# Performance work log

Hardware: AMD Instinct MI355X
Metric: run time of the kernel (lower is better)

## Reference

```python
import jax, jax.numpy as jnp
import numpy as np

PAD = 0

def setup_inputs() -> dict:
    key = jax.random.key(0)
    ks = jax.random.split(key, 16)
    B, S, D, F = 64, 512, 768, 256
    VOCAB = 32000
    # variable-length tweets: length in [8, S], rest is padding (token id PAD=0)
    lengths = jax.random.randint(ks[0], (B,), 8, S + 1)
    tok = jax.random.randint(ks[1], (B, S), 1, VOCAB)
    x = jnp.where(jnp.arange(S)[None, :] < lengths[:, None], tok, PAD)
    h = jax.random.normal(ks[2], (B, S, D), dtype=jnp.float32)
    sc = 0.02
    w2 = jax.random.normal(ks[3], (F, D, 2), dtype=jnp.float32) * sc
    b2 = jax.random.normal(ks[4], (F,), dtype=jnp.float32) * sc
    w3 = jax.random.normal(ks[5], (F, D, 3), dtype=jnp.float32) * sc
    b3 = jax.random.normal(ks[6], (F,), dtype=jnp.float32) * sc
    w4 = jax.random.normal(ks[7], (F, D, 4), dtype=jnp.float32) * sc
    b4 = jax.random.normal(ks[8], (F,), dtype=jnp.float32) * sc
    w5 = jax.random.normal(ks[9], (F, D, 5), dtype=jnp.float32) * sc
    b5 = jax.random.normal(ks[10], (F,), dtype=jnp.float32) * sc
    fc_w = jax.random.normal(ks[11], (1, 4 * F), dtype=jnp.float32) * sc
    fc_b = jax.random.normal(ks[12], (1,), dtype=jnp.float32) * sc
    return {"x": x, "h": h, "w2": w2, "b2": b2, "w3": w3, "b3": b3,
            "w4": w4, "b4": b4, "w5": w5, "b5": b5, "fc_w": fc_w, "fc_b": fc_b}


def _branch(hc, L, w, b):
    # hc: [B, D, S] front-compacted hidden states; w: [F, D, k]
    k = w.shape[-1]
    out = jax.lax.conv_general_dilated(
        hc, w, window_strides=(1,), padding='VALID',
        dimension_numbers=('NCH', 'OIH', 'NCH')) + b[None, :, None]  # [B,F,S-k+1]
    T = out.shape[-1]
    # conv position t is valid iff t + k - 1 < L  <=>  t < L - k + 1
    valid = jnp.arange(T)[None, :] < (L - k + 1)[:, None]           # [B,T]
    neg = jnp.asarray(-jnp.inf, out.dtype)
    pooled = jnp.max(jnp.where(valid[:, None, :], out, neg), axis=-1)  # [B,F]
    return jax.nn.relu(pooled)


def reference(x, h, w2, b2, w3, b3, w4, b4, w5, b5, fc_w, fc_b):
    mask = x != PAD                                   # [B,S]
    L = mask.sum(axis=1)                              # [B]
    # stable compaction: move non-pad token hidden states to the front, order preserved
    order = jnp.argsort(jnp.logical_not(mask), axis=1, stable=True)   # [B,S]
    hc = jnp.take_along_axis(h, order[..., None], axis=1)             # [B,S,D]
    hc = hc.transpose(0, 2, 1)                                        # [B,D,S]
    feats = jnp.concatenate([
        _branch(hc, L, w2, b2),
        _branch(hc, L, w3, b3),
        _branch(hc, L, w4, b4),
        _branch(hc, L, w5, b5),
    ], axis=-1)                                       # [B, 4F]
    logits = feats @ fc_w.T + fc_b                    # [B,1]
    return jax.nn.sigmoid(logits).squeeze(-1)         # [B]
```

## Files before the change

### kernel.cpp

```cpp
#include <hip/hip_runtime.h>
#include <stdint.h>

#define Bn 64
#define Sn 512
#define SPn 520
#define Dn 768
#define JSTRIDE 196608
#define ABUF 16640
#define BSLOT 8192
#define QS_A 28.222222f
#define SAQ 0.035433072f

typedef int iv4 __attribute__((ext_vector_type(4)));

static __device__ __forceinline__ signed char q8(float f, float s) {
  float t = __builtin_rintf(f * s);
  t = fmaxf(-127.f, fminf(127.f, t));
  return (signed char)(int)t;
}

static __device__ __forceinline__ void gload16(const void* g, void* l) {
  __builtin_amdgcn_global_load_lds(
      (const __attribute__((address_space(1))) unsigned int*)g,
      (__attribute__((address_space(3))) unsigned int*)l, 16, 0, 0);
}

template<int N> __device__ __forceinline__ void waitv() {
  static_assert(N == 0 || N == 1 || N == 4, "");
  if constexpr (N == 0) asm volatile("s_waitcnt vmcnt(0)" ::: "memory");
  else if constexpr (N == 1) asm volatile("s_waitcnt vmcnt(1)" ::: "memory");
  else asm volatile("s_waitcnt vmcnt(4)" ::: "memory");
}

__global__ __launch_bounds__(256) void plan_kernel(
    const int* __restrict__ x, int* __restrict__ plan, int* __restrict__ rowmap) {
  __shared__ int sL[64];
  __shared__ int sOff[65];
  int tid = threadIdx.x, lane = tid & 63, wv = tid >> 6;
  for (int bb = wv; bb < 64; bb += 4) {
    int cnt = 0;
    for (int c = 0; c < 8; ++c) {
      unsigned long long m = __ballot(x[bb * Sn + c * 64 + lane] != 0);
      cnt += __popcll(m);
    }
    if (lane == 0) sL[bb] = cnt;
  }
  __syncthreads();
  if (tid < 64) {
    int L = sL[tid];
    int SL = (L + 15) & ~15;
    int pre = SL;
    #pragma unroll
    for (int off = 1; off < 64; off <<= 1) {
      int y = __shfl_up(pre, off);
      if (tid >= off) pre += y;
    }
    sOff[tid] = pre - SL;
    if (tid == 63) { sOff[64] = pre; plan[0] = (pre + 255) >> 8; }
  }
  __syncthreads();
  int M = sOff[64];
  for (int b = 0; b < 64; ++b) {
    int off = sOff[b], L = sL[b];
    int SL = (L + 15) & ~15;
    int enc = (b << 20) | (L << 10);
    for (int t = tid; t < SL; t += 256) rowmap[off + t] = enc | t;
  }
  for (int p = M + tid; p < M + 264; p += 256)
    rowmap[p] = 512;
}

__global__ __launch_bounds__(256) void stage_kernel(
    const int* __restrict__ x, const float* __restrict__ h,
    const float* __restrict__ w2, const float* __restrict__ w3,
    const float* __restrict__ w4, const float* __restrict__ w5,
    signed char* __restrict__ hcq, signed char* __restrict__ wq,
    float* __restrict__ fscale) {
  int tid = threadIdx.x, lane = tid & 63, wv = tid >> 6;
  if (blockIdx.x < 512) {
    int cidx = blockIdx.x;
    int b = cidx >> 3, rblk = cidx & 7;
    __shared__ unsigned long long masks[8];
    __shared__ short sidx[Sn];
    for (int c = wv; c < 8; c += 4) {
      unsigned long long m = __ballot(x[b * Sn + c * 64 + lane] != 0);
      if (lane == 0) masks[c] = m;
    }
    __syncthreads();
    int pref[9]; pref[0] = 0;
    #pragma unroll
    for (int c = 0; c < 8; ++c) pref[c + 1] = pref[c] + __popcll(masks[c]);
    int L = pref[8];
    for (int p = tid; p < Sn; p += 256) {
      int c = p >> 6, l = p & 63;
      unsigned long long m = masks[c];
      if ((m >> l) & 1ull)
        sidx[pref[c] + __popcll(m & ((1ull << l) - 1ull))] = (short)p;
    }
    __syncthreads();
    int r0 = rblk * 65;
    for (int r = r0 + wv; r < r0 + 65; r += 4) {
      if (r < L) {
        signed char* dst = hcq + ((size_t)b * SPn + r) * Dn;
        const float* src = h + ((size_t)b * Sn + sidx[r]) * Dn;
        #pragma unroll
        for (int c = 0; c < 3; ++c) {
          int d = c * 256 + lane * 4;
          float4 v = *(const float4*)(src + d);
          char4 o = { q8(v.x, QS_A), q8(v.y, QS_A), q8(v.z, QS_A), q8(v.w, QS_A) };
          *(char4*)(dst + d) = o;
        }
      }
    }
  } else {
    __shared__ float sf[3840];
    __shared__ float smax[4];
    int bb = blockIdx.x - 512;
    int br = bb >> 8, f = bb & 255, k = br + 2;
    const float* w = (br == 0) ? w2 : (br == 1) ? w3 : (br == 2) ? w4 : w5;
    int mBase = 256 * ((br * (br + 3)) >> 1);
    const float* src = w + (size_t)f * Dn * k;
    int n = Dn * k;
    float mx = 0.f;
    for (int e = tid; e < n; e += 256) {
      float v = src[e];
      sf[e] = v;
      mx = fmaxf(mx, fabsf(v));
    }
    #pragma unroll
    for (int off = 32; off; off >>= 1) mx = fmaxf(mx, __shfl_xor(mx, off));
    if (lane == 0) smax[wv] = mx;
    __syncthreads();
    float M = fmaxf(fmaxf(smax[0], smax[1]), fmaxf(smax[2], smax[3]));
    M = fmaxf(M, 1e-30f);
    if (tid == 0) fscale[br * 256 + f] = M / 127.f;
    float qs = 127.f / M;
    for (int j = 0; j < k; ++j) {
      signed char* dst = wq + (size_t)(mBase + j * 256 + f) * Dn;
      for (int d = tid; d < Dn; d += 256) dst[d] = q8(sf[d * k + j], qs);
    }
  }
}

static __device__ __forceinline__ void issueA(
    int d0i, char* sA, const char* const (&gA)[2], const char* gAt,
    int lane, int wvoff) {
  int aoff = (d0i + 1) * 64;
  char* nA = sA + ((d0i + 1) & 1) * ABUF;
  #pragma unroll
  for (int p = 0; p < 2; ++p) gload16(gA[p] + aoff, nA + p * 8192 + wvoff);
  if (lane < 16) gload16(gAt + aoff, nA + 16384);
}

template<int J, int W, int J2, int DADD, int DOA>
static __device__ __forceinline__ void conv_step(
    int d0i, int bsl0, char* sA, char* sB,
    const char* const (&gA)[2], const char* gAt, const char* gB0,
    int lane, int wr, int wc, int lrow, int lg, int wvoff, iv4 (&acc)[4][4]) {
  int sl = bsl0 + J;      sl  -= (sl  >= 3) ? 3 : 0; sl  -= (sl  >= 3) ? 3 : 0;
  int dsl = bsl0 + J + 2; dsl -= (dsl >= 3) ? 3 : 0; dsl -= (dsl >= 3) ? 3 : 0;
  {
    int boff = J2 * JSTRIDE + (d0i + DADD) * 64;
    gload16(gB0 + boff, sB + dsl * BSLOT + wvoff);
  }
  if constexpr (DOA) issueA(d0i, sA, gA, gAt, lane, wvoff);
  const char* curA = sA + (d0i & 1) * ABUF;
  const char* curB = sB + sl * BSLOT;
  iv4 Af[4], Bf[4];
  #pragma unroll
  for (int m = 0; m < 4; ++m) {
    int row = wr * 64 + m * 16 + lrow + J;
    Af[m] = *(const iv4*)(curA + row * 64 + ((lg ^ ((row >> 1) & 3)) << 4));
  }
  #pragma unroll
  for (int n = 0; n < 4; ++n) {
    int row = wc * 64 + n * 16 + lrow;
    Bf[n] = *(const iv4*)(curB + row * 64 + ((lg ^ ((row >> 1) & 3)) << 4));
  }
  __builtin_amdgcn_s_setprio(1);
  #pragma unroll
  for (int n = 0; n < 4; ++n)
    #pragma unroll
    for (int m = 0; m < 4; ++m)
      acc[m][n] = __builtin_amdgcn_mfma_i32_16x16x64_i8(Af[m], Bf[n], acc[m][n], 0, 0, 0);
  __builtin_amdgcn_s_setprio(0);
  __builtin_amdgcn_sched_barrier(0);
  waitv<W>();
  __builtin_amdgcn_sched_barrier(0);
  __builtin_amdgcn_s_barrier();
  __builtin_amdgcn_sched_barrier(0);
}

#define SA bsl0, sA, sB, gA, gAt, gB0, lane, wr, wc, lrow, lg, wvoff, acc

template<int KK>
static __device__ __forceinline__ void conv_loop(
    char* sA, char* sB, const char* const (&gA)[2], const char* gAt,
    const char* gB0,
    int lane, int wr, int wc, int lrow, int lg, int wvoff, iv4 (&acc)[4][4]) {
  #pragma unroll
  for (int p = 0; p < 2; ++p) gload16(gA[p], sA + p * 8192 + wvoff);
  if (lane < 16) gload16(gAt, sA + 16384);
  gload16(gB0, sB + wvoff);
  gload16(gB0 + JSTRIDE, sB + BSLOT + wvoff);
  __builtin_amdgcn_sched_barrier(0);
  waitv<1>();
  __builtin_amdgcn_sched_barrier(0);
  __builtin_amdgcn_s_barrier();
  __builtin_amdgcn_sched_barrier(0);
  int bsl0 = 0;
  for (int d0i = 0; d0i < 11; ++d0i) {
    if constexpr (KK == 5) {
      conv_step<0,4,2,0,1>(d0i, SA);
      conv_step<1,4,3,0,0>(d0i, SA);
      conv_step<2,1,4,0,0>(d0i, SA);
      conv_step<3,1,0,1,0>(d0i, SA);
      conv_step<4,1,1,1,0>(d0i, SA);
    } else if constexpr (KK == 4) {
      conv_step<0,4,2,0,1>(d0i, SA);
      conv_step<1,4,3,0,0>(d0i, SA);
      conv_step<2,1,0,1,0>(d0i, SA);
      conv_step<3,1,1,1,0>(d0i, SA);
    } else if constexpr (KK == 3) {
      conv_step<0,4,2,0,1>(d0i, SA);
      conv_step<1,4,0,1,0>(d0i, SA);
      conv_step<2,1,1,1,0>(d0i, SA);
    } else {
      conv_step<0,4,0,1,1>(d0i, SA);
      conv_step<1,1,1,1,0>(d0i, SA);
    }
    bsl0 += KK; bsl0 -= (bsl0 >= 3) ? 3 : 0; bsl0 -= (bsl0 >= 3) ? 3 : 0;
  }
  if constexpr (KK == 5) {
    conv_step<0,1,2,0,0>(11, SA);
    conv_step<1,1,3,0,0>(11, SA);
    conv_step<2,1,4,0,0>(11, SA);
    conv_step<3,1,0,1,0>(11, SA);
    conv_step<4,1,1,1,0>(11, SA);
  } else if constexpr (KK == 4) {
    conv_step<0,1,2,0,0>(11, SA);
    conv_step<1,1,3,0,0>(11, SA);
    conv_step<2,1,0,1,0>(11, SA);
    conv_step<3,1,1,1,0>(11, SA);
  } else if constexpr (KK == 3) {
    conv_step<0,1,2,0,0>(11, SA);
    conv_step<1,1,0,1,0>(11, SA);
    conv_step<2,1,1,1,0>(11, SA);
  } else {
    conv_step<0,1,0,1,0>(11, SA);
    conv_step<1,1,1,1,0>(11, SA);
  }
  waitv<0>();
}

__global__ __launch_bounds__(512, 4) void conv_kernel(
    const signed char* __restrict__ hcq, const signed char* __restrict__ wq,
    const float* __restrict__ b2, const float* __restrict__ b3,
    const float* __restrict__ b4, const float* __restrict__ b5,
    const float* __restrict__ fscale,
    const int* __restrict__ plan, const int* __restrict__ rowmap,
    int* __restrict__ feats) {
  __shared__ char smem[2 * ABUF + 3 * BSLOT];
  char* sA = smem;
  char* sB = smem + 2 * ABUF;
  int idx = blockIdx.x;
  int xcd = idx & 7, s2 = idx >> 3;
  int sub = s2 & 7, tile = xcd + ((s2 >> 3) << 3);
  if (tile >= plan[0]) return;
  int br = 3 - (sub >> 1), ff = sub & 1, kk = br + 2;
  int mBase = 256 * ((br * (br + 3)) >> 1) + ff * 128;
  const float* bias = (br == 0) ? b2 : (br == 1) ? b3 : (br == 2) ? b4 : b5;
  int tid = threadIdx.x, lane = tid & 63, wv = tid >> 6;
  int wr = wv >> 1, wc = wv & 1;
  int lrow = lane & 15, lg = lane >> 4;
  int wvoff = wv * 1024;
  int P0 = tile << 8;

  const char* gA[2];
  #pragma unroll
  for (int p = 0; p < 2; ++p) {
    int c = p * 512 + tid;
    int row = c >> 2, sgp = c & 3;
    int rm = rowmap[P0 + row];
    int bb_ = rm >> 20, t = rm & 1023;
    int seg = sgp ^ ((row >> 1) & 3);
    gA[p] = (const char*)(hcq + ((size_t)(bb_ * SPn + t)) * Dn + seg * 16);
  }
  const char* gAt;
  {
    int l = lane & 15;
    int row = 256 + (l >> 2), sgp = l & 3;
    int rm = rowmap[P0 + row];
    int bb_ = rm >> 20, t = rm & 1023;
    int seg = sgp ^ ((row >> 1) & 3);
    gAt = (const char*)(hcq + ((size_t)(bb_ * SPn + t)) * Dn + seg * 16);
  }
  const char* gB0;
  {
    int row = tid >> 2, sgp = tid & 3;
    int seg = sgp ^ ((row >> 1) & 3);
    gB0 = (const char*)(wq + ((size_t)(mBase + row)) * Dn + seg * 16);
  }

  iv4 acc[4][4];
  #pragma unroll
  for (int m = 0; m < 4; ++m)
    #pragma unroll
    for (int n = 0; n < 4; ++n) acc[m][n] = (iv4)0;

  switch (br) {
    case 3: conv_loop<5>(sA, sB, gA, gAt, gB0, lane, wr, wc, lrow, lg, wvoff, acc); break;
    case 2: conv_loop<4>(sA, sB, gA, gAt, gB0, lane, wr, wc, lrow, lg, wvoff, acc); break;
    case 1: conv_loop<3>(sA, sB, gA, gAt, gB0, lane, wr, wc, lrow, lg, wvoff, acc); break;
    default: conv_loop<2>(sA, sB, gA, gAt, gB0, lane, wr, wc, lrow, lg, wvoff, acc); break;
  }

  int rmv[4];
  #pragma unroll
  for (int m = 0; m < 4; ++m) rmv[m] = rowmap[P0 + wr * 64 + m * 16];
  #pragma unroll
  for (int n = 0; n < 4; ++n) {
    int fg = ff * 128 + wc * 64 + n * 16 + lrow;
    float bv = bias[fg];
    float sfc = fscale[br * 256 + fg] * SAQ;
    #pragma unroll
    for (int m = 0; m < 4; ++m) {
      int bb_ = rmv[m] >> 20;
      int Lb = (rmv[m] >> 10) & 1023;
      int t0 = (rmv[m] & 1023) + lg * 4;
      int vlim = Lb - kk + 1;
      float pmax = 0.f;
      #pragma unroll
      for (int i = 0; i < 4; ++i) {
        float v = (float)acc[m][n][i] * sfc + bv;
        pmax = fmaxf(pmax, (t0 + i < vlim) ? fmaxf(v, 0.f) : 0.f);
      }
      pmax = fmaxf(pmax, __shfl_xor(pmax, 16));
      pmax = fmaxf(pmax, __shfl_xor(pmax, 32));
      if (lane < 16 && pmax > 0.f)
        atomicMax(feats + bb_ * 1024 + br * 256 + fg, __float_as_int(pmax));
    }
  }
}

__global__ __launch_bounds__(64) void fc_kernel(
    const int* __restrict__ feats, const float* __restrict__ fcw,
    const float* __restrict__ fcb, float* __restrict__ out) {
  int b = blockIdx.x, lane = threadIdx.x;
  float acc = 0.f;
  for (int i = lane; i < 1024; i += 64)
    acc += __int_as_float(feats[b * 1024 + i]) * fcw[i];
  #pragma unroll
  for (int off = 32; off; off >>= 1) acc += __shfl_xor(acc, off);
  if (lane == 0) out[b] = 1.f / (1.f + expf(-(acc + fcb[0])));
}

extern "C" void kernel_launch(void* const* d_in, const int* in_sizes, int n_in,
                              void* d_out, int out_size, void* d_ws, size_t ws_size,
                              hipStream_t stream) {
  const int*   x   = (const int*)d_in[0];
  const float* h   = (const float*)d_in[1];
  const float* w2  = (const float*)d_in[2];
  const float* b2  = (const float*)d_in[3];
  const float* w3  = (const float*)d_in[4];
  const float* b3  = (const float*)d_in[5];
  const float* w4  = (const float*)d_in[6];
  const float* b4  = (const float*)d_in[7];
  const float* w5  = (const float*)d_in[8];
  const float* b5  = (const float*)d_in[9];
  const float* fcw = (const float*)d_in[10];
  const float* fcb = (const float*)d_in[11];
  float* out = (float*)d_out;
  char* ws = (char*)d_ws;
  signed char* hcq = (signed char*)ws;
  signed char* wq  = (signed char*)(ws + 25559040);
  float* fscale = (float*)(ws + 28311552);
  int* feats  = (int*)(ws + 28315648);
  int* plan   = (int*)(ws + 28577792);
  int* rowmap = (int*)(ws + 28577808);

  hipMemsetAsync(feats, 0, 64 * 1024 * 4, stream);
  plan_kernel<<<1, 256, 0, stream>>>(x, plan, rowmap);
  stage_kernel<<<1536, 256, 0, stream>>>(x, h, w2, w3, w4, w5, hcq, wq, fscale);
  conv_kernel<<<1024, 512, 0, stream>>>(hcq, wq, b2, b3, b4, b5, fscale, plan, rowmap, feats);
  fc_kernel<<<64, 64, 0, stream>>>(feats, fcw, fcb, out);
}
```

Measured before the change: 115.2 us.

## Double-buffer register fragments and deepen B ring to four LDS slots

The conv main loop is restructured so each step prefetches the next step's A/B fragments from LDS into a second register set while the MFMAs on the current set run, and the B staging ring grows from three to four slots with power-of-two indexing. Launch bounds drop from 4 to 2 blocks per CU to make room for the extra fragment registers. Separately, the feats memset moves into plan_kernel, and weight quantization stores are vectorized to char4. The cost is more VGPRs and LDS, which may lower occupancy, in exchange for hiding LDS read latency and removing one launch.

```diff
diff --git a/kernel.cpp b/kernel.cpp
--- a/kernel.cpp
+++ b/kernel.cpp
@@ -32,11 +32,21 @@
   else asm volatile("s_waitcnt vmcnt(4)" ::: "memory");
 }
 
+template<int S, typename T, int N>
+static __device__ __forceinline__ T (&sel(T (&a)[N], T (&b)[N]))[N] {
+  if constexpr (S) return b; else return a;
+}
+
 __global__ __launch_bounds__(256) void plan_kernel(
-    const int* __restrict__ x, int* __restrict__ plan, int* __restrict__ rowmap) {
+    const int* __restrict__ x, int* __restrict__ plan, int* __restrict__ rowmap,
+    int* __restrict__ feats) {
   __shared__ int sL[64];
   __shared__ int sOff[65];
   int tid = threadIdx.x, lane = tid & 63, wv = tid >> 6;
+  {
+    int4 z = {0, 0, 0, 0};
+    for (int i = tid * 4; i < 65536; i += 1024) *(int4*)(feats + i) = z;
+  }
   for (int bb = wv; bb < 64; bb += 4) {
     int cnt = 0;
     for (int c = 0; c < 8; ++c) {
@@ -137,7 +147,11 @@
     float qs = 127.f / M;
     for (int j = 0; j < k; ++j) {
       signed char* dst = wq + (size_t)(mBase + j * 256 + f) * Dn;
-      for (int d = tid; d < Dn; d += 256) dst[d] = q8(sf[d * k + j], qs);
+      for (int d4 = tid * 4; d4 < Dn; d4 += 1024) {
+        char4 o = { q8(sf[(d4 + 0) * k + j], qs), q8(sf[(d4 + 1) * k + j], qs),
+                    q8(sf[(d4 + 2) * k + j], qs), q8(sf[(d4 + 3) * k + j], qs) };
+        *(char4*)(dst + d4) = o;
+      }
     }
   }
 }
@@ -152,31 +166,8 @@
   if (lane < 16) gload16(gAt + aoff, nA + 16384);
 }
 
-template<int J, int W, int J2, int DADD, int DOA>
-static __device__ __forceinline__ void conv_step(
-    int d0i, int bsl0, char* sA, char* sB,
-    const char* const (&gA)[2], const char* gAt, const char* gB0,
-    int lane, int wr, int wc, int lrow, int lg, int wvoff, iv4 (&acc)[4][4]) {
-  int sl = bsl0 + J;      sl  -= (sl  >= 3) ? 3 : 0; sl  -= (sl  >= 3) ? 3 : 0;
-  int dsl = bsl0 + J + 2; dsl -= (dsl >= 3) ? 3 : 0; dsl -= (dsl >= 3) ? 3 : 0;
-  {
-    int boff = J2 * JSTRIDE + (d0i + DADD) * 64;
-    gload16(gB0 + boff, sB + dsl * BSLOT + wvoff);
-  }
-  if constexpr (DOA) issueA(d0i, sA, gA, gAt, lane, wvoff);
-  const char* curA = sA + (d0i & 1) * ABUF;
-  const char* curB = sB + sl * BSLOT;
-  iv4 Af[4], Bf[4];
-  #pragma unroll
-  for (int m = 0; m < 4; ++m) {
-    int row = wr * 64 + m * 16 + lrow + J;
-    Af[m] = *(const iv4*)(curA + row * 64 + ((lg ^ ((row >> 1) & 3)) << 4));
-  }
-  #pragma unroll
-  for (int n = 0; n < 4; ++n) {
-    int row = wc * 64 + n * 16 + lrow;
-    Bf[n] = *(const iv4*)(curB + row * 64 + ((lg ^ ((row >> 1) & 3)) << 4));
-  }
+static __device__ __forceinline__ void domfma(
+    iv4 (&Af)[4], iv4 (&Bf)[4], iv4 (&acc)[4][4]) {
   __builtin_amdgcn_s_setprio(1);
   #pragma unroll
   for (int n = 0; n < 4; ++n)
@@ -184,6 +175,40 @@
     for (int m = 0; m < 4; ++m)
       acc[m][n] = __builtin_amdgcn_mfma_i32_16x16x64_i8(Af[m], Bf[n], acc[m][n], 0, 0, 0);
   __builtin_amdgcn_s_setprio(0);
+}
+
+static __device__ __forceinline__ void gates_(int W4) {}
+
+template<int J, int W, int J3, int DADD, int DOA, int SET, int PRE, int PJ, int PDADD>
+static __device__ __forceinline__ void stepN(
+    int d0i, int bsl0, char* sA, char* sB,
+    const char* const (&gA)[2], const char* gAt, const char* gB0,
+    int lane, int wr, int wc, int lrow, int lg, int wvoff,
+    iv4 (&Af0)[4], iv4 (&Bf0)[4], iv4 (&Af1)[4], iv4 (&Bf1)[4],
+    iv4 (&acc)[4][4]) {
+  {
+    int dsl = (bsl0 + J + 3) & 3;
+    gload16(gB0 + J3 * JSTRIDE + (d0i + DADD) * 64, sB + dsl * BSLOT + wvoff);
+  }
+  if constexpr (DOA) issueA(d0i, sA, gA, gAt, lane, wvoff);
+  if constexpr (PRE) {
+    int psl = (bsl0 + J + 1) & 3;
+    const char* pA = sA + ((d0i + PDADD) & 1) * ABUF;
+    const char* pB = sB + psl * BSLOT;
+    iv4 (&Afn)[4] = sel<(SET ^ 1)>(Af0, Af1);
+    iv4 (&Bfn)[4] = sel<(SET ^ 1)>(Bf0, Bf1);
+    #pragma unroll
+    for (int n = 0; n < 4; ++n) {
+      int row = wc * 64 + n * 16 + lrow;
+      Bfn[n] = *(const iv4*)(pB + row * 64 + ((lg ^ ((row >> 1) & 3)) << 4));
+    }
+    #pragma unroll
+    for (int m = 0; m < 4; ++m) {
+      int row = wr * 64 + m * 16 + lrow + PJ;
+      Afn[m] = *(const iv4*)(pA + row * 64 + ((lg ^ ((row >> 1) & 3)) << 4));
+    }
+  }
+  domfma(sel<SET>(Af0, Af1), sel<SET>(Bf0, Bf1), acc);
   __builtin_amdgcn_sched_barrier(0);
   waitv<W>();
   __builtin_amdgcn_sched_barrier(0);
@@ -191,76 +216,153 @@
   __builtin_amdgcn_sched_barrier(0);
 }
 
-#define SA bsl0, sA, sB, gA, gAt, gB0, lane, wr, wc, lrow, lg, wvoff, acc
+template<int J, int W, int J3, int DADD, int DOA, int SET, int PRE>
+static __device__ __forceinline__ void step2(
+    int d0i, int bsl0, char* sA, char* sB,
+    const char* const (&gA)[2], const char* gAt, const char* gB0,
+    int lane, int wr, int wc, int lrow, int lg, int wvoff,
+    iv4 (&Bf0)[4], iv4 (&Bf1)[4], iv4 (&acc)[4][4]) {
+  {
+    int dsl = (bsl0 + J + 3) & 3;
+    gload16(gB0 + J3 * JSTRIDE + (d0i + DADD) * 64, sB + dsl * BSLOT + wvoff);
+  }
+  if constexpr (DOA) issueA(d0i, sA, gA, gAt, lane, wvoff);
+  const char* pA = sA + (d0i & 1) * ABUF;
+  iv4 Af[4];
+  #pragma unroll
+  for (int m = 0; m < 4; ++m) {
+    int row = wr * 64 + m * 16 + lrow + J;
+    Af[m] = *(const iv4*)(pA + row * 64 + ((lg ^ ((row >> 1) & 3)) << 4));
+  }
+  if constexpr (PRE) {
+    int psl = (bsl0 + J + 1) & 3;
+    const char* pB = sB + psl * BSLOT;
+    iv4 (&Bfn)[4] = sel<(SET ^ 1)>(Bf0, Bf1);
+    #pragma unroll
+    for (int n = 0; n < 4; ++n) {
+      int row = wc * 64 + n * 16 + lrow;
+      Bfn[n] = *(const iv4*)(pB + row * 64 + ((lg ^ ((row >> 1) & 3)) << 4));
+    }
+  }
+  domfma(Af, sel<SET>(Bf0, Bf1), acc);
+  __builtin_amdgcn_sched_barrier(0);
+  waitv<W>();
+  __builtin_amdgcn_sched_barrier(0);
+  __builtin_amdgcn_s_barrier();
+  __builtin_amdgcn_sched_barrier(0);
+}
+
+#define SN bsl0, sA, sB, gA, gAt, gB0, lane, wr, wc, lrow, lg, wvoff, Af0, Bf0, Af1, Bf1, acc
+#define S2 bsl0, sA, sB, gA, gAt, gB0, lane, wr, wc, lrow, lg, wvoff, Bf0, Bf1, acc
 
 template<int KK>
 static __device__ __forceinline__ void conv_loop(
     char* sA, char* sB, const char* const (&gA)[2], const char* gAt,
     const char* gB0,
     int lane, int wr, int wc, int lrow, int lg, int wvoff, iv4 (&acc)[4][4]) {
+  iv4 Af0[4], Bf0[4], Af1[4], Bf1[4];
   #pragma unroll
   for (int p = 0; p < 2; ++p) gload16(gA[p], sA + p * 8192 + wvoff);
   if (lane < 16) gload16(gAt, sA + 16384);
   gload16(gB0, sB + wvoff);
   gload16(gB0 + JSTRIDE, sB + BSLOT + wvoff);
-  __builtin_amdgcn_sched_barrier(0);
-  waitv<1>();
+  constexpr int OFF2 = (KK >= 3) ? 2 * JSTRIDE : 64;
+  gload16(gB0 + OFF2, sB + 2 * BSLOT + wvoff);
+  __builtin_amdgcn_sched_barrier(0);
+  waitv<0>();
   __builtin_amdgcn_sched_barrier(0);
   __builtin_amdgcn_s_barrier();
   __builtin_amdgcn_sched_barrier(0);
+  {
+    #pragma unroll
+    for (int n = 0; n < 4; ++n) {
+      int row = wc * 64 + n * 16 + lrow;
+      Bf0[n] = *(const iv4*)(sB + row * 64 + ((lg ^ ((row >> 1) & 3)) << 4));
+    }
+    if constexpr (KK >= 3) {
+      #pragma unroll
+      for (int m = 0; m < 4; ++m) {
+        int row = wr * 64 + m * 16 + lrow;
+        Af0[m] = *(const iv4*)(sA + row * 64 + ((lg ^ ((row >> 1) & 3)) << 4));
+      }
+    }
+  }
   int bsl0 = 0;
-  for (int d0i = 0; d0i < 11; ++d0i) {
-    if constexpr (KK == 5) {
-      conv_step<0,4,2,0,1>(d0i, SA);
-      conv_step<1,4,3,0,0>(d0i, SA);
-      conv_step<2,1,4,0,0>(d0i, SA);
-      conv_step<3,1,0,1,0>(d0i, SA);
-      conv_step<4,1,1,1,0>(d0i, SA);
-    } else if constexpr (KK == 4) {
-      conv_step<0,4,2,0,1>(d0i, SA);
-      conv_step<1,4,3,0,0>(d0i, SA);
-      conv_step<2,1,0,1,0>(d0i, SA);
-      conv_step<3,1,1,1,0>(d0i, SA);
-    } else if constexpr (KK == 3) {
-      conv_step<0,4,2,0,1>(d0i, SA);
-      conv_step<1,4,0,1,0>(d0i, SA);
-      conv_step<2,1,1,1,0>(d0i, SA);
-    } else {
-      conv_step<0,4,0,1,1>(d0i, SA);
-      conv_step<1,1,1,1,0>(d0i, SA);
-    }
-    bsl0 += KK; bsl0 -= (bsl0 >= 3) ? 3 : 0; bsl0 -= (bsl0 >= 3) ? 3 : 0;
-  }
   if constexpr (KK == 5) {
-    conv_step<0,1,2,0,0>(11, SA);
-    conv_step<1,1,3,0,0>(11, SA);
-    conv_step<2,1,4,0,0>(11, SA);
-    conv_step<3,1,0,1,0>(11, SA);
-    conv_step<4,1,1,1,0>(11, SA);
+    for (int dd = 0; dd < 10; dd += 2) {
+      stepN<0,4,3,0,1, 0,1,1,0>(dd, SN);
+      stepN<1,4,4,0,0, 1,1,2,0>(dd, SN);
+      stepN<2,1,0,1,0, 0,1,3,0>(dd, SN);
+      stepN<3,1,1,1,0, 1,1,4,0>(dd, SN);
+      stepN<4,1,2,1,0, 0,1,0,1>(dd, SN);
+      bsl0 = (bsl0 + 5) & 3;
+      stepN<0,4,3,0,1, 1,1,1,0>(dd + 1, SN);
+      stepN<1,4,4,0,0, 0,1,2,0>(dd + 1, SN);
+      stepN<2,1,0,1,0, 1,1,3,0>(dd + 1, SN);
+      stepN<3,1,1,1,0, 0,1,4,0>(dd + 1, SN);
+      stepN<4,1,2,1,0, 1,1,0,1>(dd + 1, SN);
+      bsl0 = (bsl0 + 5) & 3;
+    }
+    stepN<0,4,3,0,1, 0,1,1,0>(10, SN);
+    stepN<1,4,4,0,0, 1,1,2,0>(10, SN);
+    stepN<2,1,0,1,0, 0,1,3,0>(10, SN);
+    stepN<3,1,1,1,0, 1,1,4,0>(10, SN);
+    stepN<4,1,2,1,0, 0,1,0,1>(10, SN);
+    bsl0 = (bsl0 + 5) & 3;
+    stepN<0,1,3,0,0, 1,1,1,0>(11, SN);
+    stepN<1,1,4,0,0, 0,1,2,0>(11, SN);
+    stepN<2,1,0,1,0, 1,1,3,0>(11, SN);
+    stepN<3,1,1,1,0, 0,1,4,0>(11, SN);
+    stepN<4,1,2,1,0, 1,0,0,0>(11, SN);
   } else if constexpr (KK == 4) {
-    conv_step<0,1,2,0,0>(11, SA);
-    conv_step<1,1,3,0,0>(11, SA);
-    conv_step<2,1,0,1,0>(11, SA);
-    conv_step<3,1,1,1,0>(11, SA);
+    for (int dd = 0; dd < 11; ++dd) {
+      stepN<0,4,3,0,1, 0,1,1,0>(dd, SN);
+      stepN<1,4,0,1,0, 1,1,2,0>(dd, SN);
+      stepN<2,1,1,1,0, 0,1,3,0>(dd, SN);
+      stepN<3,1,2,1,0, 1,1,0,1>(dd, SN);
+    }
+    stepN<0,1,3,0,0, 0,1,1,0>(11, SN);
+    stepN<1,1,0,1,0, 1,1,2,0>(11, SN);
+    stepN<2,1,1,1,0, 0,1,3,0>(11, SN);
+    stepN<3,1,2,1,0, 1,0,0,0>(11, SN);
   } else if constexpr (KK == 3) {
-    conv_step<0,1,2,0,0>(11, SA);
-    conv_step<1,1,0,1,0>(11, SA);
-    conv_step<2,1,1,1,0>(11, SA);
+    for (int dd = 0; dd < 10; dd += 2) {
+      stepN<0,4,0,1,1, 0,1,1,0>(dd, SN);
+      stepN<1,1,1,1,0, 1,1,2,0>(dd, SN);
+      stepN<2,1,2,1,0, 0,1,0,1>(dd, SN);
+      bsl0 = (bsl0 + 3) & 3;
+      stepN<0,4,0,1,1, 1,1,1,0>(dd + 1, SN);
+      stepN<1,1,1,1,0, 0,1,2,0>(dd + 1, SN);
+      stepN<2,1,2,1,0, 1,1,0,1>(dd + 1, SN);
+      bsl0 = (bsl0 + 3) & 3;
+    }
+    stepN<0,4,0,1,1, 0,1,1,0>(10, SN);
+    stepN<1,1,1,1,0, 1,1,2,0>(10, SN);
+    stepN<2,1,2,1,0, 0,1,0,1>(10, SN);
+    bsl0 = (bsl0 + 3) & 3;
+    stepN<0,1,0,1,0, 1,1,1,0>(11, SN);
+    stepN<1,1,1,1,0, 0,1,2,0>(11, SN);
+    stepN<2,1,2,1,0, 1,0,0,0>(11, SN);
   } else {
-    conv_step<0,1,0,1,0>(11, SA);
-    conv_step<1,1,1,1,0>(11, SA);
+    for (int dd = 0; dd < 11; ++dd) {
+      step2<0,4,1,1,1, 0,1>(dd, S2);
+      step2<1,1,0,2,0, 1,1>(dd, S2);
+      bsl0 = (bsl0 + 2) & 3;
+    }
+    step2<0,1,1,1,0, 0,1>(11, S2);
+    step2<1,1,0,2,0, 1,0>(11, S2);
   }
   waitv<0>();
 }
 
-__global__ __launch_bounds__(512, 4) void conv_kernel(
+__global__ __launch_bounds__(512, 2) void conv_kernel(
     const signed char* __restrict__ hcq, const signed char* __restrict__ wq,
     const float* __restrict__ b2, const float* __restrict__ b3,
     const float* __restrict__ b4, const float* __restrict__ b5,
     const float* __restrict__ fscale,
     const int* __restrict__ plan, const int* __restrict__ rowmap,
     int* __restrict__ feats) {
-  __shared__ char smem[2 * ABUF + 3 * BSLOT];
+  __shared__ char smem[2 * ABUF + 4 * BSLOT];
   char* sA = smem;
   char* sB = smem + 2 * ABUF;
   int idx = blockIdx.x;
@@ -379,8 +481,7 @@
   int* plan   = (int*)(ws + 28577792);
   int* rowmap = (int*)(ws + 28577808);
 
-  hipMemsetAsync(feats, 0, 64 * 1024 * 4, stream);
-  plan_kernel<<<1, 256, 0, stream>>>(x, plan, rowmap);
+  plan_kernel<<<1, 256, 0, stream>>>(x, plan, rowmap, feats);
   stage_kernel<<<1536, 256, 0, stream>>>(x, h, w2, w3, w4, w5, hcq, wq, fscale);
   conv_kernel<<<1024, 512, 0, stream>>>(hcq, wq, b2, b3, b4, b5, fscale, plan, rowmap, feats);
   fc_kernel<<<64, 64, 0, stream>>>(feats, fcw, fcb, out);
```

Measured after the change: 110.6 us. 1.04x faster.

## Halve conv tile rows to 128 with 256-thread blocks, fold memset into plan kernel

Applied to the files above, without the earlier changes.

The conv kernel moves from 256-row tiles with 512-thread blocks to 128-row tiles with 256-thread blocks and twice as many blocks. Each thread now issues two B loads per step, and the vmcnt wait thresholds are adjusted to match. The aim is better load balance and occupancy across CUs for the variable-length workload, at the cost of more weight reloads per output row. The hipMemsetAsync of feats is also folded into plan_kernel, and the int8 weight quantization store is vectorized to char4.

```diff
diff --git a/kernel.cpp b/kernel.cpp
--- a/kernel.cpp
+++ b/kernel.cpp
@@ -6,7 +6,7 @@
 #define SPn 520
 #define Dn 768
 #define JSTRIDE 196608
-#define ABUF 16640
+#define ABUF 8448
 #define BSLOT 8192
 #define QS_A 28.222222f
 #define SAQ 0.035433072f
@@ -26,17 +26,22 @@
 }
 
 template<int N> __device__ __forceinline__ void waitv() {
-  static_assert(N == 0 || N == 1 || N == 4, "");
+  static_assert(N == 0 || N == 2 || N == 5, "");
   if constexpr (N == 0) asm volatile("s_waitcnt vmcnt(0)" ::: "memory");
-  else if constexpr (N == 1) asm volatile("s_waitcnt vmcnt(1)" ::: "memory");
-  else asm volatile("s_waitcnt vmcnt(4)" ::: "memory");
+  else if constexpr (N == 2) asm volatile("s_waitcnt vmcnt(2)" ::: "memory");
+  else asm volatile("s_waitcnt vmcnt(5)" ::: "memory");
 }
 
 __global__ __launch_bounds__(256) void plan_kernel(
-    const int* __restrict__ x, int* __restrict__ plan, int* __restrict__ rowmap) {
+    const int* __restrict__ x, int* __restrict__ plan, int* __restrict__ rowmap,
+    int* __restrict__ feats) {
   __shared__ int sL[64];
   __shared__ int sOff[65];
   int tid = threadIdx.x, lane = tid & 63, wv = tid >> 6;
+  {
+    int4 z = {0, 0, 0, 0};
+    for (int i = tid * 4; i < 65536; i += 1024) *(int4*)(feats + i) = z;
+  }
   for (int bb = wv; bb < 64; bb += 4) {
     int cnt = 0;
     for (int c = 0; c < 8; ++c) {
@@ -56,7 +61,7 @@
       if (tid >= off) pre += y;
     }
     sOff[tid] = pre - SL;
-    if (tid == 63) { sOff[64] = pre; plan[0] = (pre + 255) >> 8; }
+    if (tid == 63) { sOff[64] = pre; plan[0] = (pre + 127) >> 7; }
   }
   __syncthreads();
   int M = sOff[64];
@@ -137,7 +142,11 @@
     float qs = 127.f / M;
     for (int j = 0; j < k; ++j) {
       signed char* dst = wq + (size_t)(mBase + j * 256 + f) * Dn;
-      for (int d = tid; d < Dn; d += 256) dst[d] = q8(sf[d * k + j], qs);
+      for (int d4 = tid * 4; d4 < Dn; d4 += 1024) {
+        char4 o = { q8(sf[(d4 + 0) * k + j], qs), q8(sf[(d4 + 1) * k + j], qs),
+                    q8(sf[(d4 + 2) * k + j], qs), q8(sf[(d4 + 3) * k + j], qs) };
+        *(char4*)(dst + d4) = o;
+      }
     }
   }
 }
@@ -147,9 +156,9 @@
     int lane, int wvoff) {
   int aoff = (d0i + 1) * 64;
   char* nA = sA + ((d0i + 1) & 1) * ABUF;
-  #pragma unroll
-  for (int p = 0; p < 2; ++p) gload16(gA[p] + aoff, nA + p * 8192 + wvoff);
-  if (lane < 16) gload16(gAt + aoff, nA + 16384);
+  gload16(gA[0] + aoff, nA + wvoff);
+  gload16(gA[1] + aoff, nA + 4096 + wvoff);
+  if (lane < 16) gload16(gAt + aoff, nA + 8192);
 }
 
 template<int J, int W, int J2, int DADD, int DOA>
@@ -161,7 +170,9 @@
   int dsl = bsl0 + J + 2; dsl -= (dsl >= 3) ? 3 : 0; dsl -= (dsl >= 3) ? 3 : 0;
   {
     int boff = J2 * JSTRIDE + (d0i + DADD) * 64;
-    gload16(gB0 + boff, sB + dsl * BSLOT + wvoff);
+    char* bdst = sB + dsl * BSLOT + wvoff;
+    gload16(gB0 + boff, bdst);
+    gload16(gB0 + 49152 + boff, bdst + 4096);
   }
   if constexpr (DOA) issueA(d0i, sA, gA, gAt, lane, wvoff);
   const char* curA = sA + (d0i & 1) * ABUF;
@@ -198,62 +209,64 @@
     char* sA, char* sB, const char* const (&gA)[2], const char* gAt,
     const char* gB0,
     int lane, int wr, int wc, int lrow, int lg, int wvoff, iv4 (&acc)[4][4]) {
-  #pragma unroll
-  for (int p = 0; p < 2; ++p) gload16(gA[p], sA + p * 8192 + wvoff);
-  if (lane < 16) gload16(gAt, sA + 16384);
+  gload16(gA[0], sA + wvoff);
+  gload16(gA[1], sA + 4096 + wvoff);
+  if (lane < 16) gload16(gAt, sA + 8192);
   gload16(gB0, sB + wvoff);
+  gload16(gB0 + 49152, sB + 4096 + wvoff);
   gload16(gB0 + JSTRIDE, sB + BSLOT + wvoff);
-  __builtin_amdgcn_sched_barrier(0);
-  waitv<1>();
+  gload16(gB0 + 49152 + JSTRIDE, sB + BSLOT + 4096 + wvoff);
+  __builtin_amdgcn_sched_barrier(0);
+  waitv<2>();
   __builtin_amdgcn_sched_barrier(0);
   __builtin_amdgcn_s_barrier();
   __builtin_amdgcn_sched_barrier(0);
   int bsl0 = 0;
   for (int d0i = 0; d0i < 11; ++d0i) {
     if constexpr (KK == 5) {
-      conv_step<0,4,2,0,1>(d0i, SA);
-      conv_step<1,4,3,0,0>(d0i, SA);
-      conv_step<2,1,4,0,0>(d0i, SA);
-      conv_step<3,1,0,1,0>(d0i, SA);
-      conv_step<4,1,1,1,0>(d0i, SA);
+      conv_step<0,5,2,0,1>(d0i, SA);
+      conv_step<1,5,3,0,0>(d0i, SA);
+      conv_step<2,2,4,0,0>(d0i, SA);
+      conv_step<3,2,0,1,0>(d0i, SA);
+      conv_step<4,2,1,1,0>(d0i, SA);
     } else if constexpr (KK == 4) {
-      conv_step<0,4,2,0,1>(d0i, SA);
-      conv_step<1,4,3,0,0>(d0i, SA);
-      conv_step<2,1,0,1,0>(d0i, SA);
-      conv_step<3,1,1,1,0>(d0i, SA);
+      conv_step<0,5,2,0,1>(d0i, SA);
+      conv_step<1,5,3,0,0>(d0i, SA);
+      conv_step<2,2,0,1,0>(d0i, SA);
+      conv_step<3,2,1,1,0>(d0i, SA);
     } else if constexpr (KK == 3) {
-      conv_step<0,4,2,0,1>(d0i, SA);
-      conv_step<1,4,0,1,0>(d0i, SA);
-      conv_step<2,1,1,1,0>(d0i, SA);
+      conv_step<0,5,2,0,1>(d0i, SA);
+      conv_step<1,5,0,1,0>(d0i, SA);
+      conv_step<2,2,1,1,0>(d0i, SA);
     } else {
-      conv_step<0,4,0,1,1>(d0i, SA);
-      conv_step<1,1,1,1,0>(d0i, SA);
+      conv_step<0,5,0,1,1>(d0i, SA);
+      conv_step<1,2,1,1,0>(d0i, SA);
     }
     bsl0 += KK; bsl0 -= (bsl0 >= 3) ? 3 : 0; bsl0 -= (bsl0 >= 3) ? 3 : 0;
   }
   if constexpr (KK == 5) {
-    conv_step<0,1,2,0,0>(11, SA);
-    conv_step<1,1,3,0,0>(11, SA);
-    conv_step<2,1,4,0,0>(11, SA);
-    conv_step<3,1,0,1,0>(11, SA);
-    conv_step<4,1,1,1,0>(11, SA);
+    conv_step<0,2,2,0,0>(11, SA);
+    conv_step<1,2,3,0,0>(11, SA);
+    conv_step<2,2,4,0,0>(11, SA);
+    conv_step<3,2,0,1,0>(11, SA);
+    conv_step<4,2,1,1,0>(11, SA);
   } else if constexpr (KK == 4) {
-    conv_step<0,1,2,0,0>(11, SA);
-    conv_step<1,1,3,0,0>(11, SA);
-    conv_step<2,1,0,1,0>(11, SA);
-    conv_step<3,1,1,1,0>(11, SA);
+    conv_step<0,2,2,0,0>(11, SA);
+    conv_step<1,2,3,0,0>(11, SA);
+    conv_step<2,2,0,1,0>(11, SA);
+    conv_step<3,2,1,1,0>(11, SA);
   } else if constexpr (KK == 3) {
-    conv_step<0,1,2,0,0>(11, SA);
-    conv_step<1,1,0,1,0>(11, SA);
-    conv_step<2,1,1,1,0>(11, SA);
+    conv_step<0,2,2,0,0>(11, SA);
+    conv_step<1,2,0,1,0>(11, SA);
+    conv_step<2,2,1,1,0>(11, SA);
   } else {
-    conv_step<0,1,0,1,0>(11, SA);
-    conv_step<1,1,1,1,0>(11, SA);
+    conv_step<0,2,0,1,0>(11, SA);
+    conv_step<1,2,1,1,0>(11, SA);
   }
   waitv<0>();
 }
 
-__global__ __launch_bounds__(512, 4) void conv_kernel(
+__global__ __launch_bounds__(256, 3) void conv_kernel(
     const signed char* __restrict__ hcq, const signed char* __restrict__ wq,
     const float* __restrict__ b2, const float* __restrict__ b3,
     const float* __restrict__ b4, const float* __restrict__ b5,
@@ -274,12 +287,12 @@
   int wr = wv >> 1, wc = wv & 1;
   int lrow = lane & 15, lg = lane >> 4;
   int wvoff = wv * 1024;
-  int P0 = tile << 8;
+  int P0 = tile << 7;
 
   const char* gA[2];
   #pragma unroll
   for (int p = 0; p < 2; ++p) {
-    int c = p * 512 + tid;
+    int c = p * 256 + tid;
     int row = c >> 2, sgp = c & 3;
     int rm = rowmap[P0 + row];
     int bb_ = rm >> 20, t = rm & 1023;
@@ -289,7 +302,7 @@
   const char* gAt;
   {
     int l = lane & 15;
-    int row = 256 + (l >> 2), sgp = l & 3;
+    int row = 128 + (l >> 2), sgp = l & 3;
     int rm = rowmap[P0 + row];
     int bb_ = rm >> 20, t = rm & 1023;
     int seg = sgp ^ ((row >> 1) & 3);
@@ -379,9 +392,8 @@
   int* plan   = (int*)(ws + 28577792);
   int* rowmap = (int*)(ws + 28577808);
 
-  hipMemsetAsync(feats, 0, 64 * 1024 * 4, stream);
-  plan_kernel<<<1, 256, 0, stream>>>(x, plan, rowmap);
+  plan_kernel<<<1, 256, 0, stream>>>(x, plan, rowmap, feats);
   stage_kernel<<<1536, 256, 0, stream>>>(x, h, w2, w3, w4, w5, hcq, wq, fscale);
-  conv_kernel<<<1024, 512, 0, stream>>>(hcq, wq, b2, b3, b4, b5, fscale, plan, rowmap, feats);
+  conv_kernel<<<2048, 256, 0, stream>>>(hcq, wq, b2, b3, b4, b5, fscale, plan, rowmap, feats);
   fc_kernel<<<64, 64, 0, stream>>>(feats, fcw, fcb, out);
 }
```

Measured after the change: 112.4 us. 2.5% less time.
